# Kernel optimization log

Measured on AMD Instinct MI355X. Metric: run time of the kernel, lower is better.

Reference implementation:

```python
import jax, jax.numpy as jnp
import numpy as np

DIM = 1024
NUM_HEADS = 16
HEAD_DIM = DIM // NUM_HEADS


def setup_inputs() -> dict:
    key = jax.random.key(0)
    ks = jax.random.split(key, 9)
    s = 1.0 / np.sqrt(DIM)
    x = jax.random.normal(ks[0], (2, 2048, DIM), dtype=jnp.float32)
    Wq = jax.random.normal(ks[1], (DIM, DIM), dtype=jnp.float32) * s
    bq = jax.random.normal(ks[2], (DIM,), dtype=jnp.float32) * s
    Wk = jax.random.normal(ks[3], (DIM, DIM), dtype=jnp.float32) * s
    bk = jax.random.normal(ks[4], (DIM,), dtype=jnp.float32) * s
    Wv = jax.random.normal(ks[5], (DIM, DIM), dtype=jnp.float32) * s
    bv = jax.random.normal(ks[6], (DIM,), dtype=jnp.float32) * s
    Wo = jax.random.normal(ks[7], (DIM, DIM), dtype=jnp.float32) * s
    bo = jax.random.normal(ks[8], (DIM,), dtype=jnp.float32) * s
    return {"x": x, "Wq": Wq, "bq": bq, "Wk": Wk, "bk": bk,
            "Wv": Wv, "bv": bv, "Wo": Wo, "bo": bo}


def _softmax_one(x, axis=-1):
    # softmax with +1 in the denominator (quiet attention)
    x = x - jnp.max(x, axis=axis, keepdims=True)
    ex = jnp.exp(x)
    return ex / (1.0 + jnp.sum(ex, axis=axis, keepdims=True))


def reference(x, Wq, bq, Wk, bk, Wv, bv, Wo, bo):
    B, L, D = x.shape
    H, hd = NUM_HEADS, HEAD_DIM
    q = (x @ Wq + bq).reshape(B, L, H, hd).transpose(0, 2, 1, 3)  # b h l d
    k = (x @ Wk + bk).reshape(B, L, H, hd).transpose(0, 2, 1, 3)
    v = (x @ Wv + bv).reshape(B, L, H, hd).transpose(0, 2, 1, 3)
    scores = jnp.einsum('bhqd,bhkd->bhqk', q, k) / np.sqrt(hd).astype(np.float32)
    # causal additive mask: -inf above the diagonal (matches torch generate_square_subsequent_mask)
    causal = jnp.triu(jnp.full((L, L), -jnp.inf, dtype=scores.dtype), k=1)
    scores = scores + causal
    attn = _softmax_one(scores, axis=-1)
    ctx = jnp.einsum('bhqk,bhkd->bhqd', attn, v)
    ctx = ctx.transpose(0, 2, 1, 3).reshape(B, L, D)
    return ctx @ Wo + bo
```

## Files before the change

kernel.cpp:

```cpp
#include <hip/hip_runtime.h>
#include <hip/hip_bf16.h>
#include <cstdint>
#include <cstddef>

#define DIMN 1024
#define NHEAD 16
#define HDIM 64
#define NB 2
#define SEQ 2048
#define MROWS 4096
#define BHN 32
#define QKV_STRIDE 4194304
#define BH_ELEMS 131072

#define QSCALE 0.18033688011112042f

typedef float f32x4 __attribute__((ext_vector_type(4)));
typedef __bf16 bf16x8 __attribute__((ext_vector_type(8)));

__device__ __forceinline__ void async_copy16(const void* g, void* l) {
    __builtin_amdgcn_global_load_lds(
        (__attribute__((address_space(1))) void*)(g),
        (__attribute__((address_space(3))) void*)(l), 16, 0, 0);
}

__device__ __forceinline__ unsigned short bf16_bits(float f) {
    __hip_bfloat16 hb = __float2bfloat16(f);
    return *(unsigned short*)&hb;
}

__device__ __forceinline__ float fast_exp2(float x) {
    return __builtin_amdgcn_exp2f(x);
}

__global__ __launch_bounds__(256) void prep_kernel(
        const float* __restrict__ x, const float* __restrict__ bq,
        const float* __restrict__ bk, const float* __restrict__ bv,
        const float* __restrict__ Wq, const float* __restrict__ Wk,
        const float* __restrict__ Wv, const float* __restrict__ Wo,
        __hip_bfloat16* __restrict__ xbf, float* __restrict__ biasq,
        __hip_bfloat16* __restrict__ wqkvt, __hip_bfloat16* __restrict__ wot) {
    __shared__ float tile[32][33];
    const int bid = blockIdx.x;
    const int t = threadIdx.x;
    if (bid < 4096) {
        int i = (bid * 256 + t) * 4;
        float4 v = *(const float4*)(x + i);
        xbf[i + 0] = __float2bfloat16(v.x);
        xbf[i + 1] = __float2bfloat16(v.y);
        xbf[i + 2] = __float2bfloat16(v.z);
        xbf[i + 3] = __float2bfloat16(v.w);
    } else if (bid < 4099) {
        int base = (bid - 4096) * 1024 + t * 4;
#pragma unroll
        for (int e = 0; e < 4; e++) {
            int gi = base + e;
            int which = gi >> 10, off = gi & 1023;
            float v = (which == 0) ? bq[off] : (which == 1) ? bk[off] : bv[off];
            biasq[gi] = v;
        }
    } else {
        int rr = bid - 4099;
        int z = rr >> 10;
        int tid = rr & 1023;
        int n0 = (tid & 31) * 32, k0 = (tid >> 5) * 32;
        const float* in = (z == 0) ? Wq : (z == 1) ? Wk : (z == 2) ? Wv : Wo;
        __hip_bfloat16* out = (z == 3) ? wot : wqkvt + (size_t)z * DIMN * DIMN;
        int tx = t & 31, ty = t >> 5;
#pragma unroll
        for (int r = 0; r < 32; r += 8)
            tile[ty + r][tx] = in[(size_t)(k0 + ty + r) * DIMN + n0 + tx];
        __syncthreads();
#pragma unroll
        for (int r = 0; r < 32; r += 8)
            out[(size_t)(n0 + ty + r) * DIMN + k0 + tx] =
                __float2bfloat16(tile[tx][ty + r]);
    }
}

__global__ __launch_bounds__(512, 1) void gemm_qkv_kernel(
        const __hip_bfloat16* __restrict__ A, const __hip_bfloat16* __restrict__ Bt,
        const float* __restrict__ bias, __hip_bfloat16* __restrict__ qkv,
        __hip_bfloat16* __restrict__ vt) {
    __shared__ __align__(16) unsigned short SM[43008];
    const int t = threadIdx.x;
    const int m0 = blockIdx.y * 256;
    const int n0 = blockIdx.x * 192;
    const int lane = t & 63;
    const int w = t >> 6;
    const int wmid = w >> 2;
    const int wnid = w & 3;
    const int r16 = lane & 15;
    const int quad = lane >> 4;
    const int rsw = (quad ^ ((r16 >> 1) & 3)) * 8;
    const bool bstage2 = (w < 4);

    const int srow = t >> 2;
    const int scsw = (t & 3) ^ ((srow >> 1) & 3);
    const __hip_bfloat16* Ag  = A  + (size_t)(m0 + srow) * DIMN + scsw * 8;
    const __hip_bfloat16* Bg1 = Bt + (size_t)(n0 + srow) * DIMN + scsw * 8;
    const __hip_bfloat16* Bg2 = Bt + (size_t)(n0 + 128 + srow) * DIMN + scsw * 8;

    f32x4 acc[8][3];
#pragma unroll
    for (int i = 0; i < 8; i++)
#pragma unroll
        for (int j = 0; j < 3; j++) acc[i][j] = (f32x4){0.f, 0.f, 0.f, 0.f};

#pragma unroll
    for (int tt = 0; tt < 2; tt++) {
#pragma unroll
        for (int h = 0; h < 2; h++)
            async_copy16(Ag + (size_t)h * 131072 + tt * 32,
                         (char*)(SM + (tt * 2 + h) * 4096 + t * 8));
        async_copy16(Bg1 + tt * 32, (char*)(SM + 24576 + tt * 6144 + t * 8));
        if (bstage2)
            async_copy16(Bg2 + tt * 32,
                         (char*)(SM + 24576 + tt * 6144 + 4096 + t * 8));
    }

    int sl = 0;
#pragma unroll 1
    for (int tt = 0; tt < 32; ++tt) {
        const int sl2 = (sl >= 1) ? (sl - 1) : 2;
        if (tt == 31) {
            asm volatile("s_waitcnt vmcnt(0)" ::: "memory");
        } else if (bstage2) {
            asm volatile("s_waitcnt vmcnt(4)" ::: "memory");
        } else {
            asm volatile("s_waitcnt vmcnt(3)" ::: "memory");
        }
        __builtin_amdgcn_s_barrier();

        const unsigned short* Asl = SM + (sl * 2 + wmid) * 4096;
        const unsigned short* Bsl = SM + 24576 + sl * 6144;

        bf16x8 af[8], bfr[3];
#pragma unroll
        for (int i = 0; i < 8; i++)
            af[i] = *(const bf16x8*)&Asl[(i * 16 + r16) * 32 + rsw];
#pragma unroll
        for (int j = 0; j < 3; j++)
            bfr[j] = *(const bf16x8*)&Bsl[(wnid * 48 + j * 16 + r16) * 32 + rsw];

        if (tt < 30) {
#pragma unroll
            for (int h = 0; h < 2; h++)
                async_copy16(Ag + (size_t)h * 131072 + (tt + 2) * 32,
                             (char*)(SM + (sl2 * 2 + h) * 4096 + t * 8));
            async_copy16(Bg1 + (tt + 2) * 32,
                         (char*)(SM + 24576 + sl2 * 6144 + t * 8));
            if (bstage2)
                async_copy16(Bg2 + (tt + 2) * 32,
                             (char*)(SM + 24576 + sl2 * 6144 + 4096 + t * 8));
        }

        __builtin_amdgcn_s_setprio(1);
#pragma unroll
        for (int i = 0; i < 8; i++)
#pragma unroll
            for (int j = 0; j < 3; j++)
                acc[i][j] = __builtin_amdgcn_mfma_f32_16x16x32_bf16(
                    af[i], bfr[j], acc[i][j], 0, 0, 0);
        __builtin_amdgcn_s_setprio(0);

        sl = (sl < 2) ? (sl + 1) : 0;
    }

#pragma unroll
    for (int j = 0; j < 3; j++) {
        const int nb = n0 + wnid * 48 + j * 16;
        const int n = nb + r16;
        const float bv = bias[n];
        const int which = nb >> 10;
        const int rem = n & 1023;
        const int hh = rem >> 6, d = rem & 63;
#pragma unroll
        for (int i = 0; i < 8; i++) {
            const int mbase = m0 + wmid * 128 + i * 16 + quad * 4;
            const int b = mbase >> 11;
            const int lrow = mbase & 2047;
            const int bh = b * NHEAD + hh;
            if (which == 2) {
                ushort4 pk;
                pk.x = bf16_bits(acc[i][j][0] + bv);
                pk.y = bf16_bits(acc[i][j][1] + bv);
                pk.z = bf16_bits(acc[i][j][2] + bv);
                pk.w = bf16_bits(acc[i][j][3] + bv);
                *(ushort4*)(vt + (size_t)bh * BH_ELEMS + (size_t)d * SEQ + lrow) = pk;
            } else {
#pragma unroll
                for (int r = 0; r < 4; r++) {
                    float v = acc[i][j][r] + bv;
                    if (which == 0) v *= QSCALE;
                    qkv[(size_t)which * QKV_STRIDE + (size_t)bh * BH_ELEMS +
                        (size_t)(lrow + r) * 64 + d] = __float2bfloat16(v);
                }
            }
        }
    }
}

__global__ __launch_bounds__(256) void gemm_out_kernel(
        const __hip_bfloat16* __restrict__ A, const __hip_bfloat16* __restrict__ Bt,
        const float* __restrict__ bias, float* __restrict__ outp) {
    __shared__ __align__(16) unsigned short As[64 * 32];
    __shared__ __align__(16) unsigned short Bs[128 * 32];
    const int t = threadIdx.x;
    const int m0 = blockIdx.y * 64;
    const int n0 = blockIdx.x * 128;
    const int lane = t & 63;
    const int w = t >> 6;
    const int wm = (w >> 1) * 32;
    const int wn = (w & 1) * 64;
    const int r16 = lane & 15;
    const int quad = lane >> 4;

    f32x4 acc[2][4];
#pragma unroll
    for (int i = 0; i < 2; i++)
#pragma unroll
        for (int j = 0; j < 4; j++) acc[i][j] = (f32x4){0.f, 0.f, 0.f, 0.f};

    const int rowA = t >> 2;
    const int kch = (t & 3) * 8;

    for (int k0 = 0; k0 < DIMN; k0 += 32) {
        __syncthreads();
        async_copy16(A + (size_t)(m0 + rowA) * DIMN + k0 + kch, (char*)As + t * 16);
#pragma unroll
        for (int r = 0; r < 2; r++) {
            int row = rowA + r * 64;
            async_copy16(Bt + (size_t)(n0 + row) * DIMN + k0 + kch,
                         (char*)Bs + (size_t)(row * 4 + (t & 3)) * 16);
        }
        __syncthreads();

        bf16x8 af[2], bfr[4];
#pragma unroll
        for (int i = 0; i < 2; i++)
            af[i] = *(const bf16x8*)&As[(wm + i * 16 + r16) * 32 + quad * 8];
#pragma unroll
        for (int j = 0; j < 4; j++)
            bfr[j] = *(const bf16x8*)&Bs[(wn + j * 16 + r16) * 32 + quad * 8];
#pragma unroll
        for (int i = 0; i < 2; i++)
#pragma unroll
            for (int j = 0; j < 4; j++)
                acc[i][j] = __builtin_amdgcn_mfma_f32_16x16x32_bf16(
                    af[i], bfr[j], acc[i][j], 0, 0, 0);
    }

#pragma unroll
    for (int i = 0; i < 2; i++)
#pragma unroll
        for (int j = 0; j < 4; j++) {
            int n = n0 + wn + j * 16 + r16;
            float bv = bias[n];
#pragma unroll
            for (int r = 0; r < 4; r++) {
                int m = m0 + wm + i * 16 + quad * 4 + r;
                outp[(size_t)m * DIMN + n] = acc[i][j][r] + bv;
            }
        }
}

__global__ __launch_bounds__(512, 4) void attn_mfma_kernel(
        const __hip_bfloat16* __restrict__ qkv, const __hip_bfloat16* __restrict__ vt,
        __hip_bfloat16* __restrict__ ctxout) {
    __shared__ __align__(16) unsigned short SMEM[36864];

    const int bx = blockIdx.x;
    const int g = bx >> 5;
    const int qt = (g < 8) ? 15 - g : g - 8;
    const int bh = bx & 31;
    const int t = threadIdx.x;
    const int lane = t & 63;
    const int w = t >> 6;
    const int half = w >> 2;
    const int wq = w & 3;
    const int r16 = lane & 15;
    const int quad = lane >> 4;
    const int qbase = qt * 128 + wq * 32;
    const int swz = quad ^ ((r16 >> 1) & 3);
    const int pkey = (r16 >> 1) & 3;

    const __hip_bfloat16* Qg = qkv + (size_t)bh * BH_ELEMS;
    const __hip_bfloat16* Kg = qkv + (size_t)QKV_STRIDE + (size_t)bh * BH_ELEMS;
    const __hip_bfloat16* Vtg = vt + (size_t)bh * BH_ELEMS;

    unsigned short* PsW = SMEM + 32768 + w * 512;

    const int cb_kp = (t & 511) >> 8;
    const int cb_rr = ((t & 511) >> 2) & 63;
    const int cb_cg = ((t & 511) & 3) ^ ((cb_rr >> 1) & 3);

    bf16x8 bq[2][2];
#pragma unroll
    for (int ng = 0; ng < 2; ng++)
#pragma unroll
        for (int kp = 0; kp < 2; kp++)
            bq[ng][kp] = *(const bf16x8*)(Qg + (size_t)(qbase + ng * 16 + r16) * 64 +
                                          kp * 32 + quad * 8);

    f32x4 oT[4][2];
#pragma unroll
    for (int mt = 0; mt < 4; mt++)
#pragma unroll
        for (int ng = 0; ng < 2; ng++) oT[mt][ng] = (f32x4){0.f, 0.f, 0.f, 0.f};
    float m_run[2] = {-1e30f, -1e30f};
    float z_run[2] = {0.f, 0.f};

    const int niter = qt + 1;

#pragma unroll
    for (int it = 0; it < 2; it++) {
        int cl = it * 512 + t;
        int ktile = (cl >> 9) ? (qt + 1) : 0;
        async_copy16(Kg + (size_t)(ktile * 64 + cb_rr) * 64 + cb_kp * 32 + cb_cg * 8,
                     (char*)SMEM + (size_t)cl * 16);
        async_copy16(Vtg + (size_t)cb_rr * SEQ + ktile * 64 + cb_kp * 32 + cb_cg * 8,
                     (char*)SMEM + 32768 + (size_t)cl * 16);
    }

#pragma unroll 1
    for (int i = 0; i < niter; i++) {
        const int curb = i & 1;
        __syncthreads();

        if (i + 1 < niter) {
            int ktA = i + 1;
            int ktB = qt + 2 + i; if (ktB > 31) ktB = 31;
#pragma unroll
            for (int it = 0; it < 2; it++) {
                int cl = it * 512 + t;
                int ktile = (cl >> 9) ? ktB : ktA;
                async_copy16(Kg + (size_t)(ktile * 64 + cb_rr) * 64 + cb_kp * 32 + cb_cg * 8,
                             (char*)SMEM + (size_t)(curb ^ 1) * 16384 + (size_t)cl * 16);
                async_copy16(Vtg + (size_t)cb_rr * SEQ + ktile * 64 + cb_kp * 32 + cb_cg * 8,
                             (char*)SMEM + 32768 + (size_t)(curb ^ 1) * 16384 + (size_t)cl * 16);
            }
        }

        const int ktile = half ? (qt + 1 + i) : i;
        const bool active = (ktile * 64 <= qbase + 31);

        if (active) {
            const unsigned short* KsW = SMEM + curb * 8192 + half * 4096;
            f32x4 st[4][2];
#pragma unroll
            for (int mt = 0; mt < 4; mt++)
#pragma unroll
                for (int ng = 0; ng < 2; ng++) st[mt][ng] = (f32x4){0.f, 0.f, 0.f, 0.f};
#pragma unroll
            for (int mt = 0; mt < 4; mt++)
#pragma unroll
                for (int kp = 0; kp < 2; kp++) {
                    bf16x8 ak = *(const bf16x8*)&KsW[kp * 2048 + (mt * 16 + r16) * 32 + swz * 8];
                    st[mt][0] = __builtin_amdgcn_mfma_f32_16x16x32_bf16(ak, bq[0][kp], st[mt][0], 0, 0, 0);
                    st[mt][1] = __builtin_amdgcn_mfma_f32_16x16x32_bf16(ak, bq[1][kp], st[mt][1], 0, 0, 0);
                }

            if (ktile * 64 + 63 > qbase) {
#pragma unroll
                for (int mt = 0; mt < 4; mt++) {
                    int kb = ktile * 64 + mt * 16 + quad * 4;
#pragma unroll
                    for (int ng = 0; ng < 2; ng++) {
                        int q = qbase + ng * 16 + r16;
#pragma unroll
                        for (int r = 0; r < 4; r++)
                            if (kb + r > q) st[mt][ng][r] = -__builtin_inff();
                    }
                }
            }

#pragma unroll
            for (int mt = 0; mt < 4; mt++)
#pragma unroll
                for (int ng = 0; ng < 2; ng++) {
                    float s0 = st[mt][ng][0], s1 = st[mt][ng][1];
                    float s2 = st[mt][ng][2], s3 = st[mt][ng][3];
                    m_run[ng] = fmaxf(m_run[ng], fmaxf(fmaxf(s0, s1), fmaxf(s2, s3)));
                    float p0 = fast_exp2(s0), p1 = fast_exp2(s1);
                    float p2 = fast_exp2(s2), p3 = fast_exp2(s3);
                    z_run[ng] += (p0 + p1) + (p2 + p3);
                    st[mt][ng][0] = p0; st[mt][ng][1] = p1;
                    st[mt][ng][2] = p2; st[mt][ng][3] = p3;
                }

            const unsigned short* VsW = SMEM + 16384 + curb * 8192 + half * 4096;
#pragma unroll
            for (int p = 0; p < 2; p++) {
#pragma unroll
                for (int ng = 0; ng < 2; ng++) {
#pragma unroll
                    for (int ml = 0; ml < 2; ml++) {
                        int mt = p * 2 + ml;
                        ushort4 pk;
                        pk.x = bf16_bits(st[mt][ng][0]);
                        pk.y = bf16_bits(st[mt][ng][1]);
                        pk.z = bf16_bits(st[mt][ng][2]);
                        pk.w = bf16_bits(st[mt][ng][3]);
                        int c = (ml * 2 + (quad >> 1)) ^ pkey;
                        *(ushort4*)&PsW[r16 * 32 + c * 8 + (quad & 1) * 4] = pk;
                    }
                    bf16x8 bp = *(const bf16x8*)&PsW[r16 * 32 + (quad ^ pkey) * 8];
#pragma unroll
                    for (int mt = 0; mt < 4; mt++) {
                        bf16x8 av = *(const bf16x8*)&VsW[p * 2048 + (mt * 16 + r16) * 32 + swz * 8];
                        oT[mt][ng] = __builtin_amdgcn_mfma_f32_16x16x32_bf16(
                            av, bp, oT[mt][ng], 0, 0, 0);
                    }
                }
            }
        }
    }

#pragma unroll
    for (int off = 16; off < 64; off <<= 1)
#pragma unroll
        for (int ng = 0; ng < 2; ng++) {
            m_run[ng] = fmaxf(m_run[ng], __shfl_xor(m_run[ng], off, 64));
            z_run[ng] += __shfl_xor(z_run[ng], off, 64);
        }

    __syncthreads();
    f32x4* CbO = (f32x4*)SMEM;
    f32x4* Ml = (f32x4*)((char*)SMEM + 32768);
    if (w >= 4) {
        int w4 = w - 4;
#pragma unroll
        for (int mt = 0; mt < 4; mt++)
#pragma unroll
            for (int ng = 0; ng < 2; ng++)
                CbO[((w4 * 8 + mt * 2 + ng) << 6) + lane] = oT[mt][ng];
        f32x4 ml;
        ml[0] = m_run[0]; ml[1] = m_run[1]; ml[2] = z_run[0]; ml[3] = z_run[1];
        Ml[(w4 << 6) + lane] = ml;
    }
    __syncthreads();
    if (w < 4) {
        f32x4 ml = Ml[(w << 6) + lane];
        float rd[2];
#pragma unroll
        for (int ng = 0; ng < 2; ng++) {
            float mtot = fmaxf(m_run[ng], ml[ng]);
            float ztot = z_run[ng] + ml[2 + ng];
            rd[ng] = 1.f / (fast_exp2(mtot) + ztot);
        }
        const int b = bh >> 4, h = bh & 15;
#pragma unroll
        for (int mt = 0; mt < 4; mt++)
#pragma unroll
            for (int ng = 0; ng < 2; ng++) {
                f32x4 O1 = CbO[((w * 8 + mt * 2 + ng) << 6) + lane];
                int q = qbase + ng * 16 + r16;
                ushort4 pk;
                pk.x = bf16_bits((oT[mt][ng][0] + O1[0]) * rd[ng]);
                pk.y = bf16_bits((oT[mt][ng][1] + O1[1]) * rd[ng]);
                pk.z = bf16_bits((oT[mt][ng][2] + O1[2]) * rd[ng]);
                pk.w = bf16_bits((oT[mt][ng][3] + O1[3]) * rd[ng]);
                *(ushort4*)(ctxout + ((size_t)(b * SEQ + q)) * DIMN + h * 64 +
                            mt * 16 + quad * 4) = pk;
            }
    }
}


extern "C" void kernel_launch(void* const* d_in, const int* in_sizes, int n_in,
                              void* d_out, int out_size, void* d_ws, size_t ws_size,
                              hipStream_t stream) {
    const float* x  = (const float*)d_in[0];
    const float* Wq = (const float*)d_in[1];
    const float* bq = (const float*)d_in[2];
    const float* Wk = (const float*)d_in[3];
    const float* bk = (const float*)d_in[4];
    const float* Wv = (const float*)d_in[5];
    const float* bv = (const float*)d_in[6];
    const float* Wo = (const float*)d_in[7];
    const float* bo = (const float*)d_in[8];

    char* ws = (char*)d_ws;
    __hip_bfloat16* xbf   = (__hip_bfloat16*)(ws);
    __hip_bfloat16* wqkvt = (__hip_bfloat16*)(ws + (8u << 20));
    __hip_bfloat16* wot   = (__hip_bfloat16*)(ws + (14u << 20));
    float*          biasq = (float*)(ws + (16u << 20));
    __hip_bfloat16* qkv   = (__hip_bfloat16*)(ws + (16u << 20) + 65536u);
    __hip_bfloat16* vt    = (__hip_bfloat16*)(ws + (16u << 20) + 65536u + (16u << 20));
    __hip_bfloat16* ctx   = (__hip_bfloat16*)(ws + (16u << 20) + 65536u + (24u << 20));
    float* out = (float*)d_out;

    prep_kernel<<<8195, 256, 0, stream>>>(x, bq, bk, bv, Wq, Wk, Wv, Wo,
                                          xbf, biasq, wqkvt, wot);
    gemm_qkv_kernel<<<dim3(16, 16), 512, 0, stream>>>(xbf, wqkvt, biasq, qkv, vt);
    attn_mfma_kernel<<<512, 512, 0, stream>>>(qkv, vt, ctx);
    gemm_out_kernel<<<dim3(8, 64), 256, 0, stream>>>(ctx, wot, bo, out);
}
```

Before: 172.4 us.

## Triple-buffer output GEMM loads with swizzled LDS layout and MFMA priority

```diff
diff --git a/kernel.cpp b/kernel.cpp
--- a/kernel.cpp
+++ b/kernel.cpp
@@ -204,8 +204,7 @@
 __global__ __launch_bounds__(256) void gemm_out_kernel(
         const __hip_bfloat16* __restrict__ A, const __hip_bfloat16* __restrict__ Bt,
         const float* __restrict__ bias, float* __restrict__ outp) {
-    __shared__ __align__(16) unsigned short As[64 * 32];
-    __shared__ __align__(16) unsigned short Bs[128 * 32];
+    __shared__ __align__(16) unsigned short SM[18432];
     const int t = threadIdx.x;
     const int m0 = blockIdx.y * 64;
     const int n0 = blockIdx.x * 128;
@@ -215,6 +214,14 @@
     const int wn = (w & 1) * 64;
     const int r16 = lane & 15;
     const int quad = lane >> 4;
+    const int rsw = (quad ^ ((r16 >> 1) & 3)) * 8;
+
+    const int srow = t >> 2;
+    const int sc = t & 3;
+    const int scswA = sc ^ ((srow >> 1) & 3);
+    const __hip_bfloat16* Ag  = A  + (size_t)(m0 + srow) * DIMN + scswA * 8;
+    const __hip_bfloat16* Bg1 = Bt + (size_t)(n0 + srow) * DIMN + scswA * 8;
+    const __hip_bfloat16* Bg2 = Bt + (size_t)(n0 + 64 + srow) * DIMN + scswA * 8;
 
     f32x4 acc[2][4];
 #pragma unroll
@@ -222,33 +229,53 @@
 #pragma unroll
         for (int j = 0; j < 4; j++) acc[i][j] = (f32x4){0.f, 0.f, 0.f, 0.f};
 
-    const int rowA = t >> 2;
-    const int kch = (t & 3) * 8;
-
-    for (int k0 = 0; k0 < DIMN; k0 += 32) {
-        __syncthreads();
-        async_copy16(A + (size_t)(m0 + rowA) * DIMN + k0 + kch, (char*)As + t * 16);
-#pragma unroll
-        for (int r = 0; r < 2; r++) {
-            int row = rowA + r * 64;
-            async_copy16(Bt + (size_t)(n0 + row) * DIMN + k0 + kch,
-                         (char*)Bs + (size_t)(row * 4 + (t & 3)) * 16);
-        }
-        __syncthreads();
+#pragma unroll
+    for (int tt = 0; tt < 2; tt++) {
+        async_copy16(Ag + tt * 32, (char*)(SM + tt * 2048 + t * 8));
+        async_copy16(Bg1 + tt * 32, (char*)(SM + 6144 + tt * 4096 + t * 8));
+        async_copy16(Bg2 + tt * 32, (char*)(SM + 6144 + tt * 4096 + 2048 + t * 8));
+    }
+
+    int sl = 0;
+#pragma unroll 1
+    for (int tt = 0; tt < 32; ++tt) {
+        const int sl2 = (sl >= 1) ? (sl - 1) : 2;
+        if (tt == 31) {
+            asm volatile("s_waitcnt vmcnt(0)" ::: "memory");
+        } else {
+            asm volatile("s_waitcnt vmcnt(3)" ::: "memory");
+        }
+        __builtin_amdgcn_s_barrier();
+
+        const unsigned short* Asl = SM + sl * 2048;
+        const unsigned short* Bsl = SM + 6144 + sl * 4096;
 
         bf16x8 af[2], bfr[4];
 #pragma unroll
         for (int i = 0; i < 2; i++)
-            af[i] = *(const bf16x8*)&As[(wm + i * 16 + r16) * 32 + quad * 8];
+            af[i] = *(const bf16x8*)&Asl[(wm + i * 16 + r16) * 32 + rsw];
 #pragma unroll
         for (int j = 0; j < 4; j++)
-            bfr[j] = *(const bf16x8*)&Bs[(wn + j * 16 + r16) * 32 + quad * 8];
+            bfr[j] = *(const bf16x8*)&Bsl[(wn + j * 16 + r16) * 32 + rsw];
+
+        if (tt < 30) {
+            async_copy16(Ag + (tt + 2) * 32, (char*)(SM + sl2 * 2048 + t * 8));
+            async_copy16(Bg1 + (tt + 2) * 32,
+                         (char*)(SM + 6144 + sl2 * 4096 + t * 8));
+            async_copy16(Bg2 + (tt + 2) * 32,
+                         (char*)(SM + 6144 + sl2 * 4096 + 2048 + t * 8));
+        }
+
+        __builtin_amdgcn_s_setprio(1);
 #pragma unroll
         for (int i = 0; i < 2; i++)
 #pragma unroll
             for (int j = 0; j < 4; j++)
                 acc[i][j] = __builtin_amdgcn_mfma_f32_16x16x32_bf16(
                     af[i], bfr[j], acc[i][j], 0, 0, 0);
+        __builtin_amdgcn_s_setprio(0);
+
+        sl = (sl < 2) ? (sl + 1) : 0;
     }
 
 #pragma unroll
```

Result: no change. 171.2 us (median of 3 runs) (-0.7%).
